# Kernel tuning notes

Measured on AMD Instinct MI355X. Metric: run time of the kernel, lower is better.

The kernel has to match this reference:

```python
import jax, jax.numpy as jnp
import numpy as np

EPS = 1e-06


def setup_inputs() -> dict:
    key = jax.random.key(0)
    ks = jax.random.split(key, 8)
    B, N, D, r, T, O, Hid = 32, 2048, 64, 32, 31, 12, 128
    in_dim = r + T  # 63
    xav = lambda k, shape: jax.random.uniform(k, shape, jnp.float32, -1.0, 1.0) * np.sqrt(6.0 / (shape[0] + shape[1]))
    return {
        "H": jax.random.normal(ks[0], (B, N, D), jnp.float32),
        "ts_out": jax.random.uniform(ks[1], (B, O, T), jnp.float32),
        "O": O,
        "P_raw": xav(ks[2], (N, r)),
        "Q_raw": xav(ks[3], (N, r)),
        "W1": xav(ks[4], (in_dim, Hid)),
        "b1": jnp.zeros((Hid,), jnp.float32),
        "W2": xav(ks[5], (Hid, r)),
        "b2": jnp.zeros((r,), jnp.float32),
        "alpha": jax.random.uniform(ks[6], (1,), jnp.float32),
    }


def reference(H, ts_out, O, P_raw, Q_raw, W1, b1, W2, b2, alpha):
    # nonnegative_basis=True -> softplus on both bases
    P = jax.nn.softplus(P_raw)  # [N, r]
    Q = jax.nn.softplus(Q_raw)  # [N, r]
    # Right contraction: U = Q^T H per batch -> [B, r, D]
    U = jnp.einsum('bnd,nr->brd', H, Q)
    # Context norm over feature dim: [B, r]
    ctx = jnp.sqrt(jnp.mean(U * U, axis=-1) + EPS)
    # Gate features: concat([ts_out [B,O,T], ctx broadcast to [B,O,r]])
    B = H.shape[0]
    ctx_exp = jnp.broadcast_to(ctx[:, None, :], (B, O, ctx.shape[-1]))
    feat = jnp.concatenate([ts_out, ctx_exp], axis=-1)  # [B, O, T+r]
    # scale MLP with exact (erf) GELU, dropout=0 (eval)
    h = jax.nn.gelu(feat @ W1 + b1, approximate=False)
    s = jax.nn.softplus(h @ W2 + b2)  # [B, O, r]
    # M = P (s \odot U) without materializing NxN: [B, O, N, D]
    M = jnp.einsum('bor,brd,nr->bond', s, U, P)
    a = jnp.clip(alpha[0], 0.0, 1.0)
    H_base = H[:, None, :, :]  # broadcast over O
    H_graph = H_base + a * (M - H_base)
    return H_graph
```

## Files before the change

kernel.cpp:

```cpp
#include <hip/hip_runtime.h>
#include <math.h>

#define B_ 32
#define N_ 2048
#define D_ 64
#define R_ 32
#define T_ 31
#define O_ 12
#define HID_ 128
#define IN_DIM_ 63
#define NCH_ 32

#define OFF_QSP   0
#define OFF_UPART (OFF_QSP + N_*R_)
#define OFF_U     (OFF_UPART + B_*NCH_*R_*D_)
#define OFF_CTX   (OFF_U + B_*R_*D_)
#define OFF_PBF   (OFF_CTX + B_*R_)
#define OFF_SUT   (OFF_PBF + N_*R_/2)

typedef __attribute__((ext_vector_type(4))) float f32x4;
typedef __attribute__((ext_vector_type(8))) short short8;

__device__ __forceinline__ float softplus_f(float x) {
    return fmaxf(x, 0.0f) + log1pf(expf(-fabsf(x)));
}
__device__ __forceinline__ float gelu_f(float x) {
    return 0.5f * x * (1.0f + erff(x * 0.70710678118654752440f));
}
__device__ __forceinline__ unsigned short f2bf(float f) {
    unsigned int u = __float_as_uint(f);
    u = (u + 0x7FFFu + ((u >> 16) & 1u)) >> 16;
    return (unsigned short)u;
}

__global__ __launch_bounds__(256) void k_softplus(const float* __restrict__ Qr,
                                                  const float* __restrict__ Pr,
                                                  float* __restrict__ ws) {
    int i = blockIdx.x * blockDim.x + threadIdx.x;
    if (i < N_ * R_) {
        ws[OFF_QSP + i] = softplus_f(Qr[i]);
    } else if (i < 2 * N_ * R_) {
        int j = i - N_ * R_;
        ((unsigned short*)(ws + OFF_PBF))[j] = f2bf(softplus_f(Pr[j]));
    }
}

__global__ __launch_bounds__(512) void k_upart(const float* __restrict__ H,
                                               float* __restrict__ ws) {
    const float* __restrict__ Qsp = ws + OFF_QSP;
    float* __restrict__ Upart = ws + OFF_UPART;
    int b = blockIdx.x / NCH_;
    int c = blockIdx.x % NCH_;
    int tid = threadIdx.x;
    int d = tid & 63;
    int rb = __builtin_amdgcn_readfirstlane(tid >> 6);
    const int r0 = rb * 4;
    float acc0 = 0.f, acc1 = 0.f, acc2 = 0.f, acc3 = 0.f;
    const int n0 = c * (N_ / NCH_);
    const float* __restrict__ Hb = H + (size_t)b * N_ * D_ + d;
    #pragma unroll 2
    for (int i = 0; i < N_ / NCH_; ++i) {
        int n = n0 + i;
        float h = Hb[(size_t)n * D_];
        const float* q = Qsp + (size_t)n * R_ + r0;
        acc0 = fmaf(h, q[0], acc0);
        acc1 = fmaf(h, q[1], acc1);
        acc2 = fmaf(h, q[2], acc2);
        acc3 = fmaf(h, q[3], acc3);
    }
    float* up = Upart + ((size_t)(b * NCH_ + c) * R_ + r0) * D_ + d;
    up[0 * D_] = acc0;
    up[1 * D_] = acc1;
    up[2 * D_] = acc2;
    up[3 * D_] = acc3;
}

__global__ __launch_bounds__(512) void k_ured(float* __restrict__ ws) {
    const float* __restrict__ Upart = ws + OFF_UPART;
    float* __restrict__ U = ws + OFF_U;
    float* __restrict__ ctx = ws + OFF_CTX;
    int b = blockIdx.x;
    int tid = threadIdx.x;
    int d = tid & 63;
    int rb = tid >> 6;
    #pragma unroll
    for (int j = 0; j < 4; ++j) {
        int r = rb * 4 + j;
        float u = 0.f;
        #pragma unroll 8
        for (int c = 0; c < NCH_; ++c)
            u += Upart[((size_t)(b * NCH_ + c) * R_ + r) * D_ + d];
        U[((size_t)b * R_ + r) * D_ + d] = u;
        float sq = u * u;
        #pragma unroll
        for (int off = 32; off; off >>= 1) sq += __shfl_xor(sq, off, 64);
        if (d == 0) ctx[b * R_ + r] = sqrtf(sq * (1.0f / D_) + 1e-6f);
    }
}

__global__ __launch_bounds__(128) void k_mlp(const float* __restrict__ ts_out,
                                             const float* __restrict__ W1,
                                             const float* __restrict__ b1,
                                             const float* __restrict__ W2,
                                             const float* __restrict__ b2,
                                             const float* __restrict__ alpha,
                                             float* __restrict__ ws) {
    __shared__ float feat[IN_DIM_];
    __shared__ float hsh[HID_];
    __shared__ float ssh[R_];
    int bo = blockIdx.x;
    int b = bo / O_;
    int tid = threadIdx.x;
    const float* __restrict__ ctx = ws + OFF_CTX;
    if (tid < T_) feat[tid] = ts_out[(size_t)bo * T_ + tid];
    else if (tid < IN_DIM_) feat[tid] = ctx[b * R_ + (tid - T_)];
    __syncthreads();
    float acc = b1[tid];
    #pragma unroll 9
    for (int k = 0; k < IN_DIM_; ++k) acc = fmaf(feat[k], W1[k * HID_ + tid], acc);
    hsh[tid] = gelu_f(acc);
    __syncthreads();
    if (tid < R_) {
        float a2 = b2[tid];
        #pragma unroll 8
        for (int j = 0; j < HID_; ++j) a2 = fmaf(hsh[j], W2[j * R_ + tid], a2);
        ssh[tid] = softplus_f(a2);
    }
    __syncthreads();
    float a = fminf(fmaxf(alpha[0], 0.0f), 1.0f);
    const float* __restrict__ U = ws + OFF_U;
    unsigned short* SUT = (unsigned short*)(ws + OFF_SUT) + (size_t)bo * D_ * R_;
    #pragma unroll
    for (int idx = tid; idx < D_ * R_; idx += 128) {
        int d = idx >> 5, r = idx & 31;
        SUT[idx] = f2bf(a * ssh[r] * U[((size_t)b * R_ + r) * D_ + d]);
    }
}

__global__ __launch_bounds__(256) void k_main(const float* __restrict__ H,
                                              const float* __restrict__ alpha,
                                              const float* __restrict__ ws,
                                              float* __restrict__ out) {
    const int b = blockIdx.y;
    const int n0 = blockIdx.x * 64 + (threadIdx.x >> 6) * 16;
    const int lane = threadIdx.x & 63;
    const int l16 = lane & 15;
    const int lhi = lane >> 4;
    const float a = fminf(fmaxf(alpha[0], 0.0f), 1.0f);
    const float oma = 1.0f - a;

    const unsigned short* Pbf = (const unsigned short*)(ws + OFF_PBF);
    const unsigned short* SUT0 = (const unsigned short*)(ws + OFF_SUT);

    short8 pfrag = *(const short8*)(Pbf + (size_t)(n0 + l16) * R_ + lhi * 8);

    const float* __restrict__ Hrow = H + ((size_t)b * N_ + n0 + l16) * D_;
    f32x4 homa[4];
    #pragma unroll
    for (int db = 0; db < 4; ++db) {
        f32x4 hv = *(const f32x4*)(Hrow + db * 16 + lhi * 4);
        homa[db] = oma * hv;
    }

    float* __restrict__ oprow = out + ((size_t)(b * O_) * N_ + n0 + l16) * D_;

    #pragma unroll 2
    for (int o = 0; o < O_; ++o) {
        const unsigned short* SUT = SUT0 + (size_t)(b * O_ + o) * D_ * R_;
        float* __restrict__ op = oprow + (size_t)o * N_ * D_;
        #pragma unroll
        for (int db = 0; db < 4; ++db) {
            short8 sfrag = *(const short8*)(SUT + (size_t)(db * 16 + l16) * R_ + lhi * 8);
            f32x4 acc = __builtin_amdgcn_mfma_f32_16x16x32_bf16(
                sfrag, pfrag, (f32x4){0.f, 0.f, 0.f, 0.f}, 0, 0, 0);
            *(f32x4*)(op + db * 16 + lhi * 4) = homa[db] + acc;
        }
    }
}

extern "C" void kernel_launch(void* const* d_in, const int* in_sizes, int n_in,
                              void* d_out, int out_size, void* d_ws, size_t ws_size,
                              hipStream_t stream) {
    const float* H      = (const float*)d_in[0];
    const float* ts_out = (const float*)d_in[1];
    const float* P_raw  = (const float*)d_in[3];
    const float* Q_raw  = (const float*)d_in[4];
    const float* W1     = (const float*)d_in[5];
    const float* b1     = (const float*)d_in[6];
    const float* W2     = (const float*)d_in[7];
    const float* b2     = (const float*)d_in[8];
    const float* alpha  = (const float*)d_in[9];
    float* out = (float*)d_out;
    float* ws  = (float*)d_ws;

    k_softplus<<<dim3((2 * N_ * R_ + 255) / 256), dim3(256), 0, stream>>>(Q_raw, P_raw, ws);
    k_upart<<<dim3(B_ * NCH_), dim3(512), 0, stream>>>(H, ws);
    k_ured<<<dim3(B_), dim3(512), 0, stream>>>(ws);
    k_mlp<<<dim3(B_ * O_), dim3(128), 0, stream>>>(ts_out, W1, b1, W2, b2, alpha, ws);
    k_main<<<dim3(N_ / 64, B_), dim3(256), 0, stream>>>(H, alpha, ws, out);
}
```

Measured before the change: 81.63 us.

## Fuse softplus into U partial kernel, split reduction grid, nontemporal output stores

Removes the separate softplus launch: each k_upart block computes softplus of its 64-row Q slice into shared memory, and batch-0 blocks also write the bf16 softplus of P. k_ured now launches B×8 blocks of 256 threads, one r per wavefront, to raise parallelism in the reduction. The main kernel's large output writes use nontemporal stores to avoid polluting the cache. In exchange, each block recomputes Q softplus redundantly across batches, and P conversion falls on only 32 blocks.

Result: slower. 107.2 us (+31.4%).

```diff
diff --git a/kernel.cpp b/kernel.cpp
--- a/kernel.cpp
+++ b/kernel.cpp
@@ -11,8 +11,7 @@
 #define IN_DIM_ 63
 #define NCH_ 32
 
-#define OFF_QSP   0
-#define OFF_UPART (OFF_QSP + N_*R_)
+#define OFF_UPART 0
 #define OFF_U     (OFF_UPART + B_*NCH_*R_*D_)
 #define OFF_CTX   (OFF_U + B_*R_*D_)
 #define OFF_PBF   (OFF_CTX + B_*R_)
@@ -33,40 +32,40 @@
     return (unsigned short)u;
 }
 
-__global__ __launch_bounds__(256) void k_softplus(const float* __restrict__ Qr,
-                                                  const float* __restrict__ Pr,
-                                                  float* __restrict__ ws) {
-    int i = blockIdx.x * blockDim.x + threadIdx.x;
-    if (i < N_ * R_) {
-        ws[OFF_QSP + i] = softplus_f(Qr[i]);
-    } else if (i < 2 * N_ * R_) {
-        int j = i - N_ * R_;
-        ((unsigned short*)(ws + OFF_PBF))[j] = f2bf(softplus_f(Pr[j]));
-    }
-}
-
 __global__ __launch_bounds__(512) void k_upart(const float* __restrict__ H,
+                                               const float* __restrict__ Qr,
+                                               const float* __restrict__ Pr,
                                                float* __restrict__ ws) {
-    const float* __restrict__ Qsp = ws + OFF_QSP;
+    __shared__ float qs[64][R_];
     float* __restrict__ Upart = ws + OFF_UPART;
     int b = blockIdx.x / NCH_;
     int c = blockIdx.x % NCH_;
     int tid = threadIdx.x;
+    const int n0 = c * 64;
+
+    #pragma unroll
+    for (int i = tid; i < 64 * R_; i += 512)
+        qs[i >> 5][i & 31] = softplus_f(Qr[(size_t)n0 * R_ + i]);
+    if (b == 0) {
+        unsigned short* Pbf = (unsigned short*)(ws + OFF_PBF);
+        #pragma unroll
+        for (int i = tid; i < 64 * R_; i += 512)
+            Pbf[(size_t)n0 * R_ + i] = f2bf(softplus_f(Pr[(size_t)n0 * R_ + i]));
+    }
+    __syncthreads();
+
     int d = tid & 63;
     int rb = __builtin_amdgcn_readfirstlane(tid >> 6);
     const int r0 = rb * 4;
     float acc0 = 0.f, acc1 = 0.f, acc2 = 0.f, acc3 = 0.f;
-    const int n0 = c * (N_ / NCH_);
-    const float* __restrict__ Hb = H + (size_t)b * N_ * D_ + d;
+    const float* __restrict__ Hb = H + ((size_t)b * N_ + n0) * D_ + d;
     #pragma unroll 2
-    for (int i = 0; i < N_ / NCH_; ++i) {
-        int n = n0 + i;
-        float h = Hb[(size_t)n * D_];
-        const float* q = Qsp + (size_t)n * R_ + r0;
-        acc0 = fmaf(h, q[0], acc0);
-        acc1 = fmaf(h, q[1], acc1);
-        acc2 = fmaf(h, q[2], acc2);
-        acc3 = fmaf(h, q[3], acc3);
+    for (int i = 0; i < 64; ++i) {
+        float h = Hb[(size_t)i * D_];
+        acc0 = fmaf(h, qs[i][r0 + 0], acc0);
+        acc1 = fmaf(h, qs[i][r0 + 1], acc1);
+        acc2 = fmaf(h, qs[i][r0 + 2], acc2);
+        acc3 = fmaf(h, qs[i][r0 + 3], acc3);
     }
     float* up = Upart + ((size_t)(b * NCH_ + c) * R_ + r0) * D_ + d;
     up[0 * D_] = acc0;
@@ -75,27 +74,22 @@
     up[3 * D_] = acc3;
 }
 
-__global__ __launch_bounds__(512) void k_ured(float* __restrict__ ws) {
+__global__ __launch_bounds__(256) void k_ured(float* __restrict__ ws) {
     const float* __restrict__ Upart = ws + OFF_UPART;
     float* __restrict__ U = ws + OFF_U;
     float* __restrict__ ctx = ws + OFF_CTX;
     int b = blockIdx.x;
-    int tid = threadIdx.x;
-    int d = tid & 63;
-    int rb = tid >> 6;
+    int r = blockIdx.y * 4 + (threadIdx.x >> 6);
+    int d = threadIdx.x & 63;
+    float u = 0.f;
+    #pragma unroll 8
+    for (int c = 0; c < NCH_; ++c)
+        u += Upart[((size_t)(b * NCH_ + c) * R_ + r) * D_ + d];
+    U[((size_t)b * R_ + r) * D_ + d] = u;
+    float sq = u * u;
     #pragma unroll
-    for (int j = 0; j < 4; ++j) {
-        int r = rb * 4 + j;
-        float u = 0.f;
-        #pragma unroll 8
-        for (int c = 0; c < NCH_; ++c)
-            u += Upart[((size_t)(b * NCH_ + c) * R_ + r) * D_ + d];
-        U[((size_t)b * R_ + r) * D_ + d] = u;
-        float sq = u * u;
-        #pragma unroll
-        for (int off = 32; off; off >>= 1) sq += __shfl_xor(sq, off, 64);
-        if (d == 0) ctx[b * R_ + r] = sqrtf(sq * (1.0f / D_) + 1e-6f);
-    }
+    for (int off = 32; off; off >>= 1) sq += __shfl_xor(sq, off, 64);
+    if (d == 0) ctx[b * R_ + r] = sqrtf(sq * (1.0f / D_) + 1e-6f);
 }
 
 __global__ __launch_bounds__(128) void k_mlp(const float* __restrict__ ts_out,
@@ -173,7 +167,7 @@
             short8 sfrag = *(const short8*)(SUT + (size_t)(db * 16 + l16) * R_ + lhi * 8);
             f32x4 acc = __builtin_amdgcn_mfma_f32_16x16x32_bf16(
                 sfrag, pfrag, (f32x4){0.f, 0.f, 0.f, 0.f}, 0, 0, 0);
-            *(f32x4*)(op + db * 16 + lhi * 4) = homa[db] + acc;
+            __builtin_nontemporal_store(homa[db] + acc, (f32x4*)(op + db * 16 + lhi * 4));
         }
     }
 }
@@ -193,9 +187,8 @@
     float* out = (float*)d_out;
     float* ws  = (float*)d_ws;
 
-    k_softplus<<<dim3((2 * N_ * R_ + 255) / 256), dim3(256), 0, stream>>>(Q_raw, P_raw, ws);
-    k_upart<<<dim3(B_ * NCH_), dim3(512), 0, stream>>>(H, ws);
-    k_ured<<<dim3(B_), dim3(512), 0, stream>>>(ws);
+    k_upart<<<dim3(B_ * NCH_), dim3(512), 0, stream>>>(H, Q_raw, P_raw, ws);
+    k_ured<<<dim3(B_, 8), dim3(256), 0, stream>>>(ws);
     k_mlp<<<dim3(B_ * O_), dim3(128), 0, stream>>>(ts_out, W1, b1, W2, b2, alpha, ws);
     k_main<<<dim3(N_ / 64, B_), dim3(256), 0, stream>>>(H, alpha, ws, out);
 }
```

## Stage main-kernel output through swizzled LDS for coalesced stores; widen reduction grid

Applied to the files above, without the earlier changes.

The main kernel now writes each MFMA result tile into an XOR-swizzled shared-memory tile, then has all threads store contiguous 16-byte chunks of the 64x64 output block. Previously each lane wrote 16-byte pieces scattered across rows. The aim is fully coalesced global writes of the large output. This adds two barriers per output slice and LDS traffic. The U-reduction kernel also gets an 8x larger grid with one r per wave, which spreads it across more CUs.

Result: faster. 73.52 us (-9.9%).

```diff
diff --git a/kernel.cpp b/kernel.cpp
--- a/kernel.cpp
+++ b/kernel.cpp
@@ -75,27 +75,22 @@
     up[3 * D_] = acc3;
 }
 
-__global__ __launch_bounds__(512) void k_ured(float* __restrict__ ws) {
+__global__ __launch_bounds__(256) void k_ured(float* __restrict__ ws) {
     const float* __restrict__ Upart = ws + OFF_UPART;
     float* __restrict__ U = ws + OFF_U;
     float* __restrict__ ctx = ws + OFF_CTX;
     int b = blockIdx.x;
-    int tid = threadIdx.x;
-    int d = tid & 63;
-    int rb = tid >> 6;
+    int r = blockIdx.y * 4 + (threadIdx.x >> 6);
+    int d = threadIdx.x & 63;
+    float u = 0.f;
+    #pragma unroll 8
+    for (int c = 0; c < NCH_; ++c)
+        u += Upart[((size_t)(b * NCH_ + c) * R_ + r) * D_ + d];
+    U[((size_t)b * R_ + r) * D_ + d] = u;
+    float sq = u * u;
     #pragma unroll
-    for (int j = 0; j < 4; ++j) {
-        int r = rb * 4 + j;
-        float u = 0.f;
-        #pragma unroll 8
-        for (int c = 0; c < NCH_; ++c)
-            u += Upart[((size_t)(b * NCH_ + c) * R_ + r) * D_ + d];
-        U[((size_t)b * R_ + r) * D_ + d] = u;
-        float sq = u * u;
-        #pragma unroll
-        for (int off = 32; off; off >>= 1) sq += __shfl_xor(sq, off, 64);
-        if (d == 0) ctx[b * R_ + r] = sqrtf(sq * (1.0f / D_) + 1e-6f);
-    }
+    for (int off = 32; off; off >>= 1) sq += __shfl_xor(sq, off, 64);
+    if (d == 0) ctx[b * R_ + r] = sqrtf(sq * (1.0f / D_) + 1e-6f);
 }
 
 __global__ __launch_bounds__(128) void k_mlp(const float* __restrict__ ts_out,
@@ -141,40 +136,53 @@
                                               const float* __restrict__ alpha,
                                               const float* __restrict__ ws,
                                               float* __restrict__ out) {
+    __shared__ float tile[64 * 64];
     const int b = blockIdx.y;
-    const int n0 = blockIdx.x * 64 + (threadIdx.x >> 6) * 16;
-    const int lane = threadIdx.x & 63;
+    const int nblk = blockIdx.x * 64;
+    const int tid = threadIdx.x;
+    const int w = tid >> 6;
+    const int lane = tid & 63;
     const int l16 = lane & 15;
     const int lhi = lane >> 4;
+    const int rl = w * 16 + l16;
     const float a = fminf(fmaxf(alpha[0], 0.0f), 1.0f);
     const float oma = 1.0f - a;
 
     const unsigned short* Pbf = (const unsigned short*)(ws + OFF_PBF);
     const unsigned short* SUT0 = (const unsigned short*)(ws + OFF_SUT);
 
-    short8 pfrag = *(const short8*)(Pbf + (size_t)(n0 + l16) * R_ + lhi * 8);
-
-    const float* __restrict__ Hrow = H + ((size_t)b * N_ + n0 + l16) * D_;
+    short8 pfrag = *(const short8*)(Pbf + (size_t)(nblk + rl) * R_ + lhi * 8);
+
+    const float* __restrict__ Hrow = H + ((size_t)b * N_ + nblk + rl) * D_;
     f32x4 homa[4];
     #pragma unroll
-    for (int db = 0; db < 4; ++db) {
-        f32x4 hv = *(const f32x4*)(Hrow + db * 16 + lhi * 4);
-        homa[db] = oma * hv;
-    }
-
-    float* __restrict__ oprow = out + ((size_t)(b * O_) * N_ + n0 + l16) * D_;
-
-    #pragma unroll 2
+    for (int db = 0; db < 4; ++db)
+        homa[db] = oma * *(const f32x4*)(Hrow + db * 16 + lhi * 4);
+
+    char* tbytes = (char*)tile;
+    float* __restrict__ oblk = out + ((size_t)(b * O_) * N_ + nblk) * D_;
+
     for (int o = 0; o < O_; ++o) {
         const unsigned short* SUT = SUT0 + (size_t)(b * O_ + o) * D_ * R_;
-        float* __restrict__ op = oprow + (size_t)o * N_ * D_;
         #pragma unroll
         for (int db = 0; db < 4; ++db) {
             short8 sfrag = *(const short8*)(SUT + (size_t)(db * 16 + l16) * R_ + lhi * 8);
-            f32x4 acc = __builtin_amdgcn_mfma_f32_16x16x32_bf16(
+            f32x4 v = homa[db] + __builtin_amdgcn_mfma_f32_16x16x32_bf16(
                 sfrag, pfrag, (f32x4){0.f, 0.f, 0.f, 0.f}, 0, 0, 0);
-            *(f32x4*)(op + db * 16 + lhi * 4) = homa[db] + acc;
+            int c = (db * 64 + lhi * 16) ^ ((rl & 7) << 4);
+            *(f32x4*)(tbytes + rl * 256 + c) = v;
         }
+        __syncthreads();
+        char* op = (char*)(oblk + (size_t)o * N_ * D_);
+        #pragma unroll
+        for (int i = 0; i < 4; ++i) {
+            int g = i * 4096 + tid * 16;
+            int rr = g >> 8;
+            int cc = (g & 255) ^ ((rr & 7) << 4);
+            f32x4 v = *(const f32x4*)(tbytes + rr * 256 + cc);
+            *(f32x4*)(op + g) = v;
+        }
+        __syncthreads();
     }
 }
 
@@ -195,7 +203,7 @@
 
     k_softplus<<<dim3((2 * N_ * R_ + 255) / 256), dim3(256), 0, stream>>>(Q_raw, P_raw, ws);
     k_upart<<<dim3(B_ * NCH_), dim3(512), 0, stream>>>(H, ws);
-    k_ured<<<dim3(B_), dim3(512), 0, stream>>>(ws);
+    k_ured<<<dim3(B_, 8), dim3(256), 0, stream>>>(ws);
     k_mlp<<<dim3(B_ * O_), dim3(128), 0, stream>>>(ts_out, W1, b1, W2, b2, alpha, ws);
     k_main<<<dim3(N_ / 64, B_), dim3(256), 0, stream>>>(H, alpha, ws, out);
 }
```
